# Optimization experiments

Hardware: AMD Instinct MI355X
Metric: run time of the kernel (lower is better)

## Reference

```python
import jax, jax.numpy as jnp
import numpy as np

N_USERS = 100000
N_ITEMS = 50000
N = N_USERS + N_ITEMS
E = 2400000
D = 64
HOPS = 3


def setup_inputs() -> dict:
    key = jax.random.key(0)
    k1, k2, k3, k4, k5 = jax.random.split(key, 5)
    user_emb = jax.random.normal(k1, (N_USERS, D), dtype=jnp.float32)
    item_emb = jax.random.normal(k2, (N_ITEMS, D), dtype=jnp.float32)
    adj_rows = jax.random.randint(k3, (E,), 0, N, dtype=jnp.int32)
    adj_cols = jax.random.randint(k4, (E,), 0, N, dtype=jnp.int32)
    # normalized-adjacency values (D^-1/2 A D^-1/2); random positives stand in
    adj_vals = jax.random.uniform(k5, (E,), dtype=jnp.float32) * 0.01
    return {
        "user_emb": user_emb,
        "item_emb": item_emb,
        "adj_rows": adj_rows,
        "adj_cols": adj_cols,
        "adj_vals": adj_vals,
        "hops": HOPS,
    }


def _spmm(rows, cols, vals, x):
    # sparse (N,N) @ dense (N,D) via gather + segment-sum
    return jax.ops.segment_sum(vals[:, None] * x[cols], rows, num_segments=N)


def reference(user_emb, item_emb, adj_rows, adj_cols, adj_vals, hops):
    ego = jnp.concatenate([user_emb, item_emb], axis=0)  # [N, D]
    acc = jnp.zeros_like(ego)
    for _ in range(hops):  # fixed small hop count
        ego = _spmm(adj_rows, adj_cols, adj_vals, ego)
        acc = acc + ego
    all_embeddings = acc / hops  # mean over stacked hop embeddings
    user_all = all_embeddings[:N_USERS]
    item_all = all_embeddings[N_USERS:]
    return (user_all, item_all)
```

## Files before the change

### kernel.cpp

```cpp
#include <hip/hip_runtime.h>

#define N_USERS 100000
#define N_ITEMS 50000
#define NN      (N_USERS + N_ITEMS)
#define DD      64
#define E_EDGES 2400000
#define HOPS    3

#define RB_BITS 7
#define RB      128
#define NBUCK   ((NN + RB - 1) >> RB_BITS)
#define CAP     2816
#define H1T     512
#define CPT     ((CAP + H1T - 1) / H1T)
#define FATB    512
#define EPB     ((E_EDGES + FATB - 1) / FATB)
#define EPT     ((EPB + 255) / 256)
#define KSC     ((NBUCK + 255) / 256)

__device__ __forceinline__ unsigned short bf16rn(float f) {
    unsigned int u = __float_as_uint(f);
    u += 0x7FFFu + ((u >> 16) & 1u);
    return (unsigned short)(u >> 16);
}
__device__ __forceinline__ float bf2f(unsigned short h) {
    return __uint_as_float((unsigned int)h << 16);
}

__device__ __forceinline__ unsigned char f8enc(float f, float cenc) {
    unsigned int s = (__float_as_uint(f) >> 31) << 7;
    float t = fabsf(f) * cenc;
    unsigned int u = __float_as_uint(t);
    u += 0x7FFFFu + ((u >> 20) & 1u);
    return (unsigned char)(((u >> 20) & 0x7F) | s);
}
__device__ __forceinline__ float f8dec(unsigned char b, float cdec) {
    unsigned int u = ((unsigned int)(b & 0x7F) << 20) |
                     ((unsigned int)(b & 0x80) << 24);
    return __uint_as_float(u) * cdec;
}

__global__ void init_cur(int* __restrict__ gcur) {
    int j = blockIdx.x * 256 + threadIdx.x;
    if (j < NBUCK) gcur[j] = j * CAP;
}

__global__ __launch_bounds__(256)
void fat_scatter(const int* __restrict__ rows,
                 const int* __restrict__ cols,
                 const float* __restrict__ vals,
                 int* __restrict__ gcur,
                 int2* __restrict__ stage) {
    __shared__ int  hist[NBUCK];
    __shared__ int  lstart[NBUCK];
    __shared__ int  gbase[NBUCK];
    __shared__ int  lcur[NBUCK];
    __shared__ int2 bin[EPB];
    __shared__ int  part[256];
    int t   = threadIdx.x;
    int off = blockIdx.x * EPB;
    int cnt = min(EPB, E_EDGES - off);

    for (int j = t; j < NBUCK; j += 256) hist[j] = 0;
    __syncthreads();

    int rreg[EPT];
    for (int k = 0; k < EPT; ++k) {
        int i = t + k * 256;
        if (i < cnt) {
            int r = rows[off + i];
            rreg[k] = r;
            atomicAdd(&hist[r >> RB_BITS], 1);
        }
    }
    __syncthreads();

    int loc[KSC];
    int sum = 0;
    for (int k = 0; k < KSC; ++k) {
        int j = t * KSC + k;
        int v = (j < NBUCK) ? hist[j] : 0;
        loc[k] = sum;
        sum += v;
    }
    part[t] = sum;
    __syncthreads();
    for (int o = 1; o < 256; o <<= 1) {
        int v = (t >= o) ? part[t - o] : 0;
        __syncthreads();
        part[t] += v;
        __syncthreads();
    }
    int pre = part[t] - sum;
    for (int k = 0; k < KSC; ++k) {
        int j = t * KSC + k;
        if (j < NBUCK) { lstart[j] = pre + loc[k]; lcur[j] = pre + loc[k]; }
    }
    __syncthreads();

    for (int j = t; j < NBUCK; j += 256) {
        int n = hist[j];
        gbase[j] = n ? atomicAdd(&gcur[j], n) : 0;
    }

    for (int k = 0; k < EPT; ++k) {
        int i = t + k * 256;
        if (i < cnt) {
            int r = rreg[k];
            int c = cols[off + i];
            float v = vals[off + i];
            int p = atomicAdd(&lcur[r >> RB_BITS], 1);
            bin[p] = make_int2(((r & (RB - 1)) << 18) | c, __float_as_int(v));
        }
    }
    __syncthreads();

    for (int j = t; j < NBUCK; j += 256) {
        int n = hist[j];
        if (!n) continue;
        int ls = lstart[j];
        int gd = gbase[j];
        for (int k = 0; k < n; ++k) stage[gd + k] = bin[ls + k];
    }
}

__global__ void scan_counts(const int* __restrict__ gcur, int* __restrict__ ebase) {
    __shared__ int part[256];
    int t = threadIdx.x;
    int loc[KSC];
    int sum = 0;
    for (int k = 0; k < KSC; ++k) {
        int j = t * KSC + k;
        int v = (j < NBUCK) ? (gcur[j] - j * CAP) : 0;
        loc[k] = sum;
        sum += v;
    }
    part[t] = sum;
    __syncthreads();
    for (int o = 1; o < 256; o <<= 1) {
        int v = (t >= o) ? part[t - o] : 0;
        __syncthreads();
        part[t] += v;
        __syncthreads();
    }
    int pre = part[t] - sum;
    for (int k = 0; k < KSC; ++k) {
        int j = t * KSC + k;
        if (j < NBUCK) ebase[j] = pre + loc[k];
    }
}

__global__ void conv_bf16(const float4* __restrict__ user4,
                          const float4* __restrict__ item4,
                          ushort4* __restrict__ x0) {
    const int n4 = NN * DD / 4;
    const int u4 = N_USERS * DD / 4;
    int i = blockIdx.x * 256 + threadIdx.x;
    if (i >= n4) return;
    float4 v = (i < u4) ? user4[i] : item4[i - u4];
    ushort4 o;
    o.x = bf16rn(v.x); o.y = bf16rn(v.y);
    o.z = bf16rn(v.z); o.w = bf16rn(v.w);
    x0[i] = o;
}

__global__ __launch_bounds__(H1T, 4)
void hop1_sort_spmm(const int* __restrict__ gcur,
                    const int* __restrict__ ebase,
                    const int2* __restrict__ stage,
                    int2* __restrict__ ep,
                    int* __restrict__ row_ptr,
                    const unsigned short* __restrict__ x,
                    unsigned short* __restrict__ ybf,
                    unsigned char* __restrict__ yf8) {
    __shared__ int2 bin[CAP];
    __shared__ int  hist[RB];
    __shared__ int  sc[RB];
    __shared__ int  rstart[RB + 1];
    __shared__ int  rcur[RB];
    int b = blockIdx.x;
    int t = threadIdx.x;
    int cnt = min(gcur[b] - b * CAP, CAP);
    const int2* src = stage + (size_t)b * CAP;

    if (t < RB) hist[t] = 0;
    __syncthreads();

    int2 ereg[CPT];
    for (int k = 0; k < CPT; ++k) {
        int i = t + k * H1T;
        if (i < cnt) {
            int2 p = src[i];
            ereg[k] = p;
            atomicAdd(&hist[p.x >> 18], 1);
        }
    }
    __syncthreads();

    int hv = 0;
    if (t < RB) { hv = hist[t]; sc[t] = hv; }
    __syncthreads();
    for (int o = 1; o < RB; o <<= 1) {
        int v = 0;
        if (t < RB && t >= o) v = sc[t - o];
        __syncthreads();
        if (t < RB) sc[t] += v;
        __syncthreads();
    }
    if (t < RB) {
        int ex = sc[t] - hv;
        rstart[t] = ex;
        rcur[t]   = ex;
    }
    if (t == 0) rstart[RB] = cnt;
    __syncthreads();

    for (int k = 0; k < CPT; ++k) {
        int i = t + k * H1T;
        if (i < cnt) {
            int2 p = ereg[k];
            int pos = atomicAdd(&rcur[p.x >> 18], 1);
            bin[pos] = p;
        }
    }
    __syncthreads();

    int eb = ebase[b];
    for (int i = t; i < cnt; i += H1T)
        ep[eb + i] = make_int2(bin[i].x & 0x3FFFF, bin[i].y);
    if (t < RB) {
        int row = (b << RB_BITS) + t;
        if (row <= NN) row_ptr[row] = eb + rstart[t];
    }

    int lane = t & 63;
    int w    = t >> 6;
    int qid  = lane >> 4;
    unsigned fb = (unsigned)(lane & 15) << 3;
    const char* xb = (const char*)x;
    for (int lr = w * 16; lr < w * 16 + 16; ++lr) {
        int row = (b << RB_BITS) + lr;
        if (row >= NN) continue;
        int s  = rstart[lr];
        int en = rstart[lr + 1];
        float s0 = 0.f, s1 = 0.f, s2 = 0.f, s3 = 0.f;
        int e = s;
        for (; e + 16 <= en; e += 16) {
            int2 pe[4];
#pragma unroll
            for (int k = 0; k < 4; ++k) pe[k] = bin[e + 4 * k + qid];
            uint2 g[4];
#pragma unroll
            for (int k = 0; k < 4; ++k) {
                unsigned off = ((unsigned)(pe[k].x & 0x3FFFF) << 7) + fb;
                g[k] = *(const uint2*)(xb + off);
            }
#pragma unroll
            for (int k = 0; k < 4; ++k) {
                float wv = __int_as_float(pe[k].y);
                s0 += wv * __uint_as_float(g[k].x << 16);
                s1 += wv * __uint_as_float(g[k].x & 0xffff0000u);
                s2 += wv * __uint_as_float(g[k].y << 16);
                s3 += wv * __uint_as_float(g[k].y & 0xffff0000u);
            }
        }
        if (e < en) {
            int last = en - 1;
            int2 pe[4];
            int idx[4];
#pragma unroll
            for (int k = 0; k < 4; ++k) {
                idx[k] = e + 4 * k + qid;
                pe[k] = bin[min(idx[k], last)];
            }
            uint2 g[4];
#pragma unroll
            for (int k = 0; k < 4; ++k) {
                unsigned off = ((unsigned)(pe[k].x & 0x3FFFF) << 7) + fb;
                g[k] = *(const uint2*)(xb + off);
            }
#pragma unroll
            for (int k = 0; k < 4; ++k) {
                float wv = (idx[k] <= last) ? __int_as_float(pe[k].y) : 0.f;
                s0 += wv * __uint_as_float(g[k].x << 16);
                s1 += wv * __uint_as_float(g[k].x & 0xffff0000u);
                s2 += wv * __uint_as_float(g[k].y << 16);
                s3 += wv * __uint_as_float(g[k].y & 0xffff0000u);
            }
        }
        s0 += __shfl_xor(s0, 16); s0 += __shfl_xor(s0, 32);
        s1 += __shfl_xor(s1, 16); s1 += __shfl_xor(s1, 32);
        s2 += __shfl_xor(s2, 16); s2 += __shfl_xor(s2, 32);
        s3 += __shfl_xor(s3, 16); s3 += __shfl_xor(s3, 32);
        if (qid == 0) {
            int o = row * DD + (int)(fb >> 1);
            ushort4 ob;
            ob.x = bf16rn(s0); ob.y = bf16rn(s1);
            ob.z = bf16rn(s2); ob.w = bf16rn(s3);
            *(ushort4*)(ybf + o) = ob;
            uchar4 of;
            of.x = f8enc(s0, 0x1p-114f); of.y = f8enc(s1, 0x1p-114f);
            of.z = f8enc(s2, 0x1p-114f); of.w = f8enc(s3, 0x1p-114f);
            *(uchar4*)(yf8 + o) = of;
        }
    }
}

__global__ __launch_bounds__(256)
void spmm_h2(const int* __restrict__ row_ptr,
             const int2* __restrict__ ep,
             const unsigned char* __restrict__ xf8,
             unsigned short* __restrict__ ybf,
             unsigned char* __restrict__ yf8) {
    int r = blockIdx.x * 4 + (threadIdx.x >> 6);
    if (r >= NN) return;
    r = __builtin_amdgcn_readfirstlane(r);
    int lane = threadIdx.x & 63;
    int s  = row_ptr[r];
    int en = row_ptr[r + 1];
    float sum = 0.f;
    int e = s;
    for (; e + 16 <= en; e += 16) {
        int2 pe[16];
#pragma unroll
        for (int k = 0; k < 16; ++k) pe[k] = ep[e + k];
        float g[16];
#pragma unroll
        for (int k = 0; k < 16; ++k)
            g[k] = f8dec(xf8[(size_t)pe[k].x * DD + lane], 0x1p114f);
#pragma unroll
        for (int k = 0; k < 16; ++k)
            sum += __int_as_float(pe[k].y) * g[k];
    }
    if (e < en) {
        int last = en - 1;
        int2 pe[16];
#pragma unroll
        for (int k = 0; k < 16; ++k) pe[k] = ep[min(e + k, last)];
        float g[16];
#pragma unroll
        for (int k = 0; k < 16; ++k)
            g[k] = f8dec(xf8[(size_t)pe[k].x * DD + lane], 0x1p114f);
#pragma unroll
        for (int k = 0; k < 16; ++k) {
            float w = (e + k <= last) ? __int_as_float(pe[k].y) : 0.f;
            sum += w * g[k];
        }
    }
    int o = r * DD + lane;
    ybf[o] = bf16rn(sum);
    yf8[o] = f8enc(sum, 0x1p-109f);
}

__global__ __launch_bounds__(256)
void spmm_h3_fin(const int* __restrict__ row_ptr,
                 const int2* __restrict__ ep,
                 const unsigned char* __restrict__ xf8,
                 const unsigned short* __restrict__ y1bf,
                 const unsigned short* __restrict__ y2bf,
                 float* __restrict__ acc) {
    int r = blockIdx.x * 4 + (threadIdx.x >> 6);
    if (r >= NN) return;
    r = __builtin_amdgcn_readfirstlane(r);
    int lane = threadIdx.x & 63;
    int s  = row_ptr[r];
    int en = row_ptr[r + 1];
    float sum = 0.f;
    int e = s;
    for (; e + 16 <= en; e += 16) {
        int2 pe[16];
#pragma unroll
        for (int k = 0; k < 16; ++k) pe[k] = ep[e + k];
        float g[16];
#pragma unroll
        for (int k = 0; k < 16; ++k)
            g[k] = f8dec(xf8[(size_t)pe[k].x * DD + lane], 0x1p109f);
#pragma unroll
        for (int k = 0; k < 16; ++k)
            sum += __int_as_float(pe[k].y) * g[k];
    }
    if (e < en) {
        int last = en - 1;
        int2 pe[16];
#pragma unroll
        for (int k = 0; k < 16; ++k) pe[k] = ep[min(e + k, last)];
        float g[16];
#pragma unroll
        for (int k = 0; k < 16; ++k)
            g[k] = f8dec(xf8[(size_t)pe[k].x * DD + lane], 0x1p109f);
#pragma unroll
        for (int k = 0; k < 16; ++k) {
            float w = (e + k <= last) ? __int_as_float(pe[k].y) : 0.f;
            sum += w * g[k];
        }
    }
    int o = r * DD + lane;
    float y1v = bf2f(y1bf[o]);
    float y2v = bf2f(y2bf[o]);
    acc[o] = (y1v + y2v + sum) * (1.0f / 3.0f);
}

extern "C" void kernel_launch(void* const* d_in, const int* in_sizes, int n_in,
                              void* d_out, int out_size, void* d_ws, size_t ws_size,
                              hipStream_t stream) {
    const float* user_emb = (const float*)d_in[0];
    const float* item_emb = (const float*)d_in[1];
    const int*   adj_rows = (const int*)d_in[2];
    const int*   adj_cols = (const int*)d_in[3];
    const float* adj_vals = (const float*)d_in[4];

    float* acc = (float*)d_out;

    int2*           stage   = (int2*)d_ws;
    int2*           ep      = stage + (size_t)NBUCK * CAP;
    unsigned short* x0      = (unsigned short*)(ep + E_EDGES);
    unsigned short* y1bf    = x0 + (size_t)NN * DD;
    unsigned char*  y1f8    = (unsigned char*)(y1bf + (size_t)NN * DD);
    int*            row_ptr = (int*)(y1f8 + (size_t)NN * DD);
    int*            gcur    = row_ptr + NN + 1;
    int*            ebase   = gcur + NBUCK;
    unsigned short* y2bf    = x0;
    unsigned char*  y2f8    = (unsigned char*)stage;

    const int tpb = 256;
    const int grid_r = (NN + 3) / 4;
    const int grid_c = (NN * DD / 4 + tpb - 1) / tpb;
    (void)ws_size; (void)in_sizes; (void)n_in; (void)out_size;

    init_cur<<<(NBUCK + tpb - 1) / tpb, tpb, 0, stream>>>(gcur);
    fat_scatter<<<FATB, tpb, 0, stream>>>(adj_rows, adj_cols, adj_vals,
                                          gcur, stage);
    scan_counts<<<1, tpb, 0, stream>>>(gcur, ebase);
    conv_bf16<<<grid_c, tpb, 0, stream>>>((const float4*)user_emb,
                                          (const float4*)item_emb,
                                          (ushort4*)x0);

    hop1_sort_spmm<<<NBUCK, H1T, 0, stream>>>(gcur, ebase, stage, ep, row_ptr,
                                              x0, y1bf, y1f8);
    spmm_h2<<<grid_r, tpb, 0, stream>>>(row_ptr, ep, y1f8, y2bf, y2f8);
    spmm_h3_fin<<<grid_r, tpb, 0, stream>>>(row_ptr, ep, y2f8, y1bf, y2bf, acc);
}
```

Baseline: 368.0 us.

## Gather four fp8 features per lane across quarter-wave edge groups in hops 2-3

Hop-2 and hop-3 SpMM kernels now split each wavefront into four 16-lane groups. Each group handles a different edge, and each lane loads a 4-byte word holding four fp8 features instead of one byte per lane. The partial sums are combined with cross-lane shuffles, and one quarter-wave writes vectorised outputs. The aim is fewer, wider gather loads and a cheaper inline fp8 decode, at the cost of shuffle reductions and 16 edges per iteration spread across groups.

```diff
diff --git a/kernel.cpp b/kernel.cpp
--- a/kernel.cpp
+++ b/kernel.cpp
@@ -316,40 +316,66 @@
     if (r >= NN) return;
     r = __builtin_amdgcn_readfirstlane(r);
     int lane = threadIdx.x & 63;
+    int qid  = lane >> 4;
+    unsigned fb = (unsigned)(lane & 15) << 2;
     int s  = row_ptr[r];
     int en = row_ptr[r + 1];
-    float sum = 0.f;
+    float s0 = 0.f, s1 = 0.f, s2 = 0.f, s3 = 0.f;
     int e = s;
     for (; e + 16 <= en; e += 16) {
-        int2 pe[16];
-#pragma unroll
-        for (int k = 0; k < 16; ++k) pe[k] = ep[e + k];
-        float g[16];
-#pragma unroll
-        for (int k = 0; k < 16; ++k)
-            g[k] = f8dec(xf8[(size_t)pe[k].x * DD + lane], 0x1p114f);
-#pragma unroll
-        for (int k = 0; k < 16; ++k)
-            sum += __int_as_float(pe[k].y) * g[k];
+        int2 pe[4];
+#pragma unroll
+        for (int k = 0; k < 4; ++k) pe[k] = ep[e + 4 * k + qid];
+        unsigned g[4];
+#pragma unroll
+        for (int k = 0; k < 4; ++k)
+            g[k] = *(const unsigned*)(xf8 + (((unsigned)pe[k].x << 6) + fb));
+#pragma unroll
+        for (int k = 0; k < 4; ++k) {
+            float wvc = __int_as_float(pe[k].y) * 0x1p114f;
+            s0 += wvc * __uint_as_float(((g[k] & 0x7Fu)       << 20) | ((g[k] & 0x80u)       << 24));
+            s1 += wvc * __uint_as_float(((g[k] & 0x7F00u)     << 12) | ((g[k] & 0x8000u)     << 16));
+            s2 += wvc * __uint_as_float(((g[k] & 0x7F0000u)   <<  4) | ((g[k] & 0x800000u)   <<  8));
+            s3 += wvc * __uint_as_float(((g[k] & 0x7F000000u) >>  4) |  (g[k] & 0x80000000u));
+        }
     }
     if (e < en) {
         int last = en - 1;
-        int2 pe[16];
-#pragma unroll
-        for (int k = 0; k < 16; ++k) pe[k] = ep[min(e + k, last)];
-        float g[16];
-#pragma unroll
-        for (int k = 0; k < 16; ++k)
-            g[k] = f8dec(xf8[(size_t)pe[k].x * DD + lane], 0x1p114f);
-#pragma unroll
-        for (int k = 0; k < 16; ++k) {
-            float w = (e + k <= last) ? __int_as_float(pe[k].y) : 0.f;
-            sum += w * g[k];
-        }
-    }
-    int o = r * DD + lane;
-    ybf[o] = bf16rn(sum);
-    yf8[o] = f8enc(sum, 0x1p-109f);
+        int2 pe[4];
+        int idx[4];
+#pragma unroll
+        for (int k = 0; k < 4; ++k) {
+            idx[k] = e + 4 * k + qid;
+            pe[k] = ep[min(idx[k], last)];
+        }
+        unsigned g[4];
+#pragma unroll
+        for (int k = 0; k < 4; ++k)
+            g[k] = *(const unsigned*)(xf8 + (((unsigned)pe[k].x << 6) + fb));
+#pragma unroll
+        for (int k = 0; k < 4; ++k) {
+            float wvc = (idx[k] <= last) ? __int_as_float(pe[k].y) * 0x1p114f : 0.f;
+            s0 += wvc * __uint_as_float(((g[k] & 0x7Fu)       << 20) | ((g[k] & 0x80u)       << 24));
+            s1 += wvc * __uint_as_float(((g[k] & 0x7F00u)     << 12) | ((g[k] & 0x8000u)     << 16));
+            s2 += wvc * __uint_as_float(((g[k] & 0x7F0000u)   <<  4) | ((g[k] & 0x800000u)   <<  8));
+            s3 += wvc * __uint_as_float(((g[k] & 0x7F000000u) >>  4) |  (g[k] & 0x80000000u));
+        }
+    }
+    s0 += __shfl_xor(s0, 16); s0 += __shfl_xor(s0, 32);
+    s1 += __shfl_xor(s1, 16); s1 += __shfl_xor(s1, 32);
+    s2 += __shfl_xor(s2, 16); s2 += __shfl_xor(s2, 32);
+    s3 += __shfl_xor(s3, 16); s3 += __shfl_xor(s3, 32);
+    if (qid == 0) {
+        int o = r * DD + (int)fb;
+        ushort4 ob;
+        ob.x = bf16rn(s0); ob.y = bf16rn(s1);
+        ob.z = bf16rn(s2); ob.w = bf16rn(s3);
+        *(ushort4*)(ybf + o) = ob;
+        uchar4 of;
+        of.x = f8enc(s0, 0x1p-109f); of.y = f8enc(s1, 0x1p-109f);
+        of.z = f8enc(s2, 0x1p-109f); of.w = f8enc(s3, 0x1p-109f);
+        *(uchar4*)(yf8 + o) = of;
+    }
 }
 
 __global__ __launch_bounds__(256)
@@ -363,41 +389,66 @@
     if (r >= NN) return;
     r = __builtin_amdgcn_readfirstlane(r);
     int lane = threadIdx.x & 63;
+    int qid  = lane >> 4;
+    unsigned fb = (unsigned)(lane & 15) << 2;
     int s  = row_ptr[r];
     int en = row_ptr[r + 1];
-    float sum = 0.f;
+    float s0 = 0.f, s1 = 0.f, s2 = 0.f, s3 = 0.f;
     int e = s;
     for (; e + 16 <= en; e += 16) {
-        int2 pe[16];
-#pragma unroll
-        for (int k = 0; k < 16; ++k) pe[k] = ep[e + k];
-        float g[16];
-#pragma unroll
-        for (int k = 0; k < 16; ++k)
-            g[k] = f8dec(xf8[(size_t)pe[k].x * DD + lane], 0x1p109f);
-#pragma unroll
-        for (int k = 0; k < 16; ++k)
-            sum += __int_as_float(pe[k].y) * g[k];
+        int2 pe[4];
+#pragma unroll
+        for (int k = 0; k < 4; ++k) pe[k] = ep[e + 4 * k + qid];
+        unsigned g[4];
+#pragma unroll
+        for (int k = 0; k < 4; ++k)
+            g[k] = *(const unsigned*)(xf8 + (((unsigned)pe[k].x << 6) + fb));
+#pragma unroll
+        for (int k = 0; k < 4; ++k) {
+            float wvc = __int_as_float(pe[k].y) * 0x1p109f;
+            s0 += wvc * __uint_as_float(((g[k] & 0x7Fu)       << 20) | ((g[k] & 0x80u)       << 24));
+            s1 += wvc * __uint_as_float(((g[k] & 0x7F00u)     << 12) | ((g[k] & 0x8000u)     << 16));
+            s2 += wvc * __uint_as_float(((g[k] & 0x7F0000u)   <<  4) | ((g[k] & 0x800000u)   <<  8));
+            s3 += wvc * __uint_as_float(((g[k] & 0x7F000000u) >>  4) |  (g[k] & 0x80000000u));
+        }
     }
     if (e < en) {
         int last = en - 1;
-        int2 pe[16];
-#pragma unroll
-        for (int k = 0; k < 16; ++k) pe[k] = ep[min(e + k, last)];
-        float g[16];
-#pragma unroll
-        for (int k = 0; k < 16; ++k)
-            g[k] = f8dec(xf8[(size_t)pe[k].x * DD + lane], 0x1p109f);
-#pragma unroll
-        for (int k = 0; k < 16; ++k) {
-            float w = (e + k <= last) ? __int_as_float(pe[k].y) : 0.f;
-            sum += w * g[k];
-        }
-    }
-    int o = r * DD + lane;
-    float y1v = bf2f(y1bf[o]);
-    float y2v = bf2f(y2bf[o]);
-    acc[o] = (y1v + y2v + sum) * (1.0f / 3.0f);
+        int2 pe[4];
+        int idx[4];
+#pragma unroll
+        for (int k = 0; k < 4; ++k) {
+            idx[k] = e + 4 * k + qid;
+            pe[k] = ep[min(idx[k], last)];
+        }
+        unsigned g[4];
+#pragma unroll
+        for (int k = 0; k < 4; ++k)
+            g[k] = *(const unsigned*)(xf8 + (((unsigned)pe[k].x << 6) + fb));
+#pragma unroll
+        for (int k = 0; k < 4; ++k) {
+            float wvc = (idx[k] <= last) ? __int_as_float(pe[k].y) * 0x1p109f : 0.f;
+            s0 += wvc * __uint_as_float(((g[k] & 0x7Fu)       << 20) | ((g[k] & 0x80u)       << 24));
+            s1 += wvc * __uint_as_float(((g[k] & 0x7F00u)     << 12) | ((g[k] & 0x8000u)     << 16));
+            s2 += wvc * __uint_as_float(((g[k] & 0x7F0000u)   <<  4) | ((g[k] & 0x800000u)   <<  8));
+            s3 += wvc * __uint_as_float(((g[k] & 0x7F000000u) >>  4) |  (g[k] & 0x80000000u));
+        }
+    }
+    s0 += __shfl_xor(s0, 16); s0 += __shfl_xor(s0, 32);
+    s1 += __shfl_xor(s1, 16); s1 += __shfl_xor(s1, 32);
+    s2 += __shfl_xor(s2, 16); s2 += __shfl_xor(s2, 32);
+    s3 += __shfl_xor(s3, 16); s3 += __shfl_xor(s3, 32);
+    if (qid == 0) {
+        int o = r * DD + (int)fb;
+        ushort4 y1 = *(const ushort4*)(y1bf + o);
+        ushort4 y2 = *(const ushort4*)(y2bf + o);
+        float4 ov;
+        ov.x = (bf2f(y1.x) + bf2f(y2.x) + s0) * (1.0f / 3.0f);
+        ov.y = (bf2f(y1.y) + bf2f(y2.y) + s1) * (1.0f / 3.0f);
+        ov.z = (bf2f(y1.z) + bf2f(y2.z) + s2) * (1.0f / 3.0f);
+        ov.w = (bf2f(y1.w) + bf2f(y2.w) + s3) * (1.0f / 3.0f);
+        *(float4*)(acc + o) = ov;
+    }
 }
 
 extern "C" void kernel_launch(void* const* d_in, const int* in_sizes, int n_in,
```

New measurement: 361.7 us. About the same (-1.7%).
